# Performance work log

Measured on AMD Instinct MI355X. Metric: run time of the kernel, lower is better.

The kernel has to match this reference:

```python
import jax, jax.numpy as jnp
import numpy as np
from jax import lax

N, S, H, L, E, V = 10000, 20, 512, 2, 100000, 10000


def setup_inputs() -> dict:
    key = jax.random.key(0)
    ks = jax.random.split(key, 12)
    return {
        "emb": jax.random.normal(ks[0], (V, H), jnp.float32),
        "W_ir": jax.random.normal(ks[1], (L, H, H), jnp.float32) * (2.0 / H) ** 0.5,
        "b_ir": jnp.ones((L, H), jnp.float32),
        "W_iz": jax.random.normal(ks[2], (L, H, H), jnp.float32) * (2.0 / H) ** 0.5,
        "b_iz": jnp.ones((L, H), jnp.float32),
        "lin_w": jax.random.normal(ks[3], (1, H), jnp.float32) * (1.0 / H) ** 0.5,
        "lin_b": jnp.zeros((1,), jnp.float32),
        "skip_w": jax.random.uniform(ks[4], (H, H), jnp.float32),
        "skip_b": jax.random.uniform(ks[5], (H,), jnp.float32),
        "walk_idx": jax.random.randint(ks[6], (N, S), 0, V),
        "edge_label_index": jax.random.randint(ks[7], (2, E), 0, N),
    }


def reference(emb, W_ir, b_ir, W_iz, b_iz, lin_w, lin_b, skip_w, skip_b,
              walk_idx, edge_label_index):
    x = emb[walk_idx]                       # [N, S, H]
    hn = jnp.zeros((x.shape[0], emb.shape[1]), x.dtype)
    for l in range(W_ir.shape[0]):
        # gates depend only on x, precompute all steps: F.linear(x, W) = x @ W.T
        h_all = jnp.einsum('nsh,kh->snk', x, W_ir[l]) + b_ir[l]          # [S, N, H]
        z_all = jax.nn.sigmoid(jnp.einsum('nsh,kh->snk', x, W_iz[l]) + b_iz[l])

        def step(h, tz):
            ht, zt = tz
            return (1.0 - zt) * h + zt * ht, None

        hn, _ = lax.scan(step, hn, (h_all, z_all))
    # note: F.dropout result in original is dead (overwritten); omitted
    score = jax.nn.sigmoid(hn @ lin_w.T + lin_b)        # [N, 1]
    node_feat = score[edge_label_index]                  # [2, E, 1]
    pred = jnp.sum(node_feat[0] * node_feat[1], axis=-1)  # [E] ('dot' decode)
    out2 = hn @ skip_w.T + skip_b                        # [N, H]
    return pred, out2
```

## Files before the change

kernel.cpp:

```cpp
#include <hip/hip_runtime.h>

#define H  512
#define NN 10000
#define SS 20
#define VV 100000
#define EE 100000

typedef __bf16 bf16x8 __attribute__((ext_vector_type(8)));
typedef float  f32x4  __attribute__((ext_vector_type(4)));

__device__ __forceinline__ unsigned short f2bf(float f) {
  unsigned u = __builtin_bit_cast(unsigned, f);
  u += 0x7FFFu + ((u >> 16) & 1u);
  return (unsigned short)(u >> 16);
}
__device__ __forceinline__ float bflo(int x) {
  return __builtin_bit_cast(float, (unsigned)x << 16);
}
__device__ __forceinline__ float bfhi(int x) {
  return __builtin_bit_cast(float, (unsigned)x & 0xFFFF0000u);
}
__device__ __forceinline__ float sigm(float x) { return 1.f / (1.f + __expf(-x)); }

__device__ __forceinline__ unsigned pk(float lo, float hi) {
  unsigned a = __builtin_bit_cast(unsigned, lo) + 0x8000u;
  unsigned b = __builtin_bit_cast(unsigned, hi) + 0x8000u;
  return __builtin_amdgcn_perm(b, a, 0x07060302u);
}
__device__ __forceinline__ void cvt_store8(unsigned short* dst, float4 a, float4 b) {
  int4 v;
  v.x = (int)pk(a.x, a.y); v.y = (int)pk(a.z, a.w);
  v.z = (int)pk(b.x, b.y); v.w = (int)pk(b.z, b.w);
  *(int4*)dst = v;
}
__device__ __forceinline__ bf16x8 cvt8(float4 a, float4 b) {
  int4 v;
  v.x = (int)pk(a.x, a.y); v.y = (int)pk(a.z, a.w);
  v.z = (int)pk(b.x, b.y); v.w = (int)pk(b.z, b.w);
  return __builtin_bit_cast(bf16x8, v);
}

__launch_bounds__(256, 2)
__global__ void gru_fused(const float* __restrict__ emb,
                          const float* __restrict__ W_ir,
                          const float* __restrict__ W_iz,
                          const float* __restrict__ b_ir,
                          const float* __restrict__ b_iz,
                          const int* __restrict__ walk,
                          unsigned short* __restrict__ hnb) {
  __shared__ unsigned short As[2][80 * 64];
  __shared__ unsigned short hout[2][4][32];

  const int tid = threadIdx.x;
  const int w = tid >> 6, lane = tid & 63;
  const int r = lane & 15, q = lane >> 4;

  const int hwid = blockIdx.y * 16 + blockIdx.x;
  const int cg = (hwid >> 3) & 15;
  const int sb = ((hwid & 7) << 3) + (hwid >> 7);
  const int c0 = cg * 32;

  const int ly = r & 1;
  const int cch = c0 + 8 * w + (r >> 1);
  bf16x8 barr[2][16];
  float bias2[2];
  #pragma unroll
  for (int t = 0; t < 2; ++t) {
    const float* wrow = (t ? W_iz : W_ir) + (long)ly * H * H + (long)cch * H;
    #pragma unroll
    for (int u = 0; u < 16; ++u) {
      const float* s = wrow + u * 32 + q * 8;
      barr[t][u] = cvt8(*(const float4*)s, *(const float4*)(s + 4));
    }
    bias2[t] = (t ? b_iz : b_ir)[ly * H + cch];
  }

  const int row0 = tid >> 3, g0 = tid & 7;
  const int row1 = row0 + 32, row2 = row0 + 64;
  const bool has2 = (tid < 128);
  #define LMAP(m) (20 * (((m) >> 2) & 3) + 4 * ((m) >> 4) + ((m) & 3))
  #define SWZ(m)  ((m) * 64 + ((g0 ^ ((m) & 7)) * 8))
  const int L0 = LMAP(row0), L1 = LMAP(row1), L2 = LMAP(row2);
  const int sw0 = SWZ(row0), sw1 = SWZ(row1), sw2 = SWZ(row2);

  const int ngA = (2500 * sb) >> 6;
  const int ngB = (2500 * (sb + 1)) >> 6;

  int v0 = walk[ngA * 80 + L0]; v0 = ((unsigned)v0 < VV) ? v0 : 0;
  int v1 = walk[ngA * 80 + L1]; v1 = ((unsigned)v1 < VV) ? v1 : 0;
  int cur0 = v0 * H, cur1 = v1 * H, cur2 = 0;
  if (has2) { int v2 = walk[ngA * 80 + L2]; v2 = ((unsigned)v2 < VV) ? v2 : 0; cur2 = v2 * H; }

  float4 pa0, pb0, pa1, pb1, pa2 = {0,0,0,0}, pb2 = {0,0,0,0};
  {
    const float* s0 = emb + cur0 + g0 * 8;
    pa0 = *(const float4*)s0; pb0 = *(const float4*)(s0 + 4);
    const float* s1 = emb + cur1 + g0 * 8;
    pa1 = *(const float4*)s1; pb1 = *(const float4*)(s1 + 4);
    if (has2) { const float* s2 = emb + cur2 + g0 * 8;
                pa2 = *(const float4*)s2; pb2 = *(const float4*)(s2 + 4); }
  }

  f32x4 acc[5][2];
  const f32x4 fz = {0.f, 0.f, 0.f, 0.f};

  for (int ng = ngA; ng < ngB; ++ng) {
    #pragma unroll
    for (int mt = 0; mt < 5; ++mt)
      #pragma unroll
      for (int t = 0; t < 2; ++t) acc[mt][t] = fz;

    const int ngn = (ng + 1 < ngB) ? ng + 1 : ng;
    int n0 = walk[ngn * 80 + L0]; n0 = ((unsigned)n0 < VV) ? n0 : 0;
    int n1 = walk[ngn * 80 + L1]; n1 = ((unsigned)n1 < VV) ? n1 : 0;
    const int nxt0 = n0 * H, nxt1 = n1 * H;
    int nxt2 = 0;
    if (has2) { int n2 = walk[ngn * 80 + L2]; n2 = ((unsigned)n2 < VV) ? n2 : 0; nxt2 = n2 * H; }

    #pragma unroll
    for (int kc = 0; kc < 8; ++kc) {
      unsigned short* Ab = &As[kc & 1][0];
      cvt_store8(&Ab[sw0], pa0, pb0);
      cvt_store8(&Ab[sw1], pa1, pb1);
      if (has2) cvt_store8(&Ab[sw2], pa2, pb2);
      __syncthreads();
      {
        const int ko = (kc < 7) ? (kc + 1) * 64 : 0;
        const int o0 = (kc < 7) ? cur0 : nxt0;
        const int o1 = (kc < 7) ? cur1 : nxt1;
        const int o2 = (kc < 7) ? cur2 : nxt2;
        const float* s0 = emb + o0 + ko + g0 * 8;
        pa0 = *(const float4*)s0; pb0 = *(const float4*)(s0 + 4);
        const float* s1 = emb + o1 + ko + g0 * 8;
        pa1 = *(const float4*)s1; pb1 = *(const float4*)(s1 + 4);
        if (has2) { const float* s2 = emb + o2 + ko + g0 * 8;
                    pa2 = *(const float4*)s2; pb2 = *(const float4*)(s2 + 4); }
      }
      #pragma unroll
      for (int ks = 0; ks < 2; ++ks) {
        bf16x8 a[5];
        #pragma unroll
        for (int mt = 0; mt < 5; ++mt) {
          const int ar = mt * 16 + r;
          a[mt] = *(const bf16x8*)&Ab[ar * 64 + (((ks * 4 + q) ^ (ar & 7)) * 8)];
        }
        #pragma unroll
        for (int mt = 0; mt < 5; ++mt)
          #pragma unroll
          for (int t = 0; t < 2; ++t)
            acc[mt][t] = __builtin_amdgcn_mfma_f32_16x16x32_bf16(
                a[mt], barr[t][kc * 2 + ks], acc[mt][t], 0, 0, 0);
      }
    }

    {
      float hn1 = 0.f, a2 = 1.f, b2 = 0.f;
      #pragma unroll
      for (int s = 0; s < 20; ++s) {
        const float yh = acc[s >> 2][0][s & 3] + bias2[0];
        const float yz = acc[s >> 2][1][s & 3] + bias2[1];
        const float z = sigm(yz);
        hn1 += z * (yh - hn1);
        a2 *= (1.f - z);
        b2 += z * (yh - b2);
      }
      const float u2 = __shfl_xor(hn1, 1);
      if (ly == 1) hout[ng & 1][q][8 * w + (r >> 1)] = f2bf(a2 * u2 + b2);
    }
    __syncthreads();
    if (tid < 16) {
      const int nd = tid >> 2, seg = tid & 3;
      int4 v = *(const int4*)&hout[ng & 1][nd][seg * 8];
      *(int4*)(hnb + (long)(ng * 4 + nd) * 1024 + c0 + seg * 8) = v;
    }
    cur0 = nxt0; cur1 = nxt1; cur2 = nxt2;
  }
}

__global__ void score_kernel(const unsigned short* __restrict__ hnb,
                             const float* __restrict__ lin_w,
                             const float* __restrict__ lin_b,
                             float* __restrict__ R) {
  int tid = threadIdx.x;
  int wv = tid >> 6, lane = tid & 63;
  int node = blockIdx.x * 4 + wv;
  int k = lane * 8;
  int4 hv = *(const int4*)(hnb + (long)node * 1024 + k);
  float4 w0 = *(const float4*)(lin_w + k);
  float4 w1 = *(const float4*)(lin_w + k + 4);
  float s = bflo(hv.x) * w0.x + bfhi(hv.x) * w0.y + bflo(hv.y) * w0.z + bfhi(hv.y) * w0.w
          + bflo(hv.z) * w1.x + bfhi(hv.z) * w1.y + bflo(hv.w) * w1.z + bfhi(hv.w) * w1.w;
  #pragma unroll
  for (int off = 32; off > 0; off >>= 1) s += __shfl_down(s, off);
  if (lane == 0) R[256 + (long)node * 512] = sigm(s + lin_b[0]);
}

__global__ void pred_kernel(const int* __restrict__ eli, const float* __restrict__ R,
                            float* __restrict__ out) {
  int e = blockIdx.x * 256 + threadIdx.x;
  if (e < EE) {
    int a = eli[e];       a = (unsigned)a < NN ? a : 0;
    int b = eli[EE + e];  b = (unsigned)b < NN ? b : 0;
    out[e] = R[256 + (long)a * 512] * R[256 + (long)b * 512];
  }
}

__launch_bounds__(256)
__global__ void out2_kernel(const unsigned short* __restrict__ hnb,
                            const float* __restrict__ skip_w,
                            const float* __restrict__ skip_b,
                            float* __restrict__ out2) {
  __shared__ unsigned short Asl[32][520];
  __shared__ unsigned short Bsl[512][40];
  const int tid = threadIdx.x;
  const int lane = tid & 63, wv = tid >> 6;
  const int r = lane & 15, q = lane >> 4;
  const int m0 = blockIdx.x * 32;

  {
    int arow = tid >> 4;
    int acol = (tid & 15) * 32;
    #pragma unroll
    for (int hh = 0; hh < 2; ++hh) {
      int grow = m0 + hh * 16 + arow;
      unsigned short* dst = &Asl[hh * 16 + arow][acol];
      if (grow < NN) {
        const unsigned short* hr = hnb + (long)grow * 1024 + acol;
        *(int4*)(dst)      = *(const int4*)(hr);
        *(int4*)(dst + 8)  = *(const int4*)(hr + 8);
        *(int4*)(dst + 16) = *(const int4*)(hr + 16);
        *(int4*)(dst + 24) = *(const int4*)(hr + 24);
      } else {
        int4 z = {0, 0, 0, 0};
        *(int4*)(dst) = z; *(int4*)(dst + 8) = z;
        *(int4*)(dst + 16) = z; *(int4*)(dst + 24) = z;
      }
    }
  }

  const f32x4 fzero = {0.f, 0.f, 0.f, 0.f};
  f32x4 acc[2][8];
  #pragma unroll
  for (int rg = 0; rg < 2; ++rg)
    #pragma unroll
    for (int i = 0; i < 8; ++i) acc[rg][i] = fzero;

  const int ksub = (tid & 3) * 8;
  const int jb = tid >> 2;

  for (int k0 = 0; k0 < H; k0 += 32) {
    __syncthreads();
    #pragma unroll
    for (int it = 0; it < 8; ++it) {
      int jj = it * 64 + jb;
      const float* src = skip_w + (long)jj * H + k0 + ksub;
      cvt_store8(&Bsl[jj][ksub], *(const float4*)src, *(const float4*)(src + 4));
    }
    __syncthreads();
    bf16x8 af0 = *(const bf16x8*)&Asl[r][k0 + q * 8];
    bf16x8 af1 = *(const bf16x8*)&Asl[16 + r][k0 + q * 8];
    #pragma unroll
    for (int i = 0; i < 8; ++i) {
      bf16x8 bf = *(const bf16x8*)&Bsl[(wv * 8 + i) * 16 + r][q * 8];
      acc[0][i] = __builtin_amdgcn_mfma_f32_16x16x32_bf16(af0, bf, acc[0][i], 0, 0, 0);
      acc[1][i] = __builtin_amdgcn_mfma_f32_16x16x32_bf16(af1, bf, acc[1][i], 0, 0, 0);
    }
  }
  #pragma unroll
  for (int rg = 0; rg < 2; ++rg)
    #pragma unroll
    for (int i = 0; i < 8; ++i) {
      int col = (wv * 8 + i) * 16 + r;
      float sbv = skip_b[col];
      #pragma unroll
      for (int g = 0; g < 4; ++g) {
        int grow = m0 + rg * 16 + q * 4 + g;
        if (grow < NN) out2[(long)grow * H + col] = acc[rg][i][g] + sbv;
      }
    }
}

extern "C" void kernel_launch(void* const* d_in, const int* in_sizes, int n_in,
                              void* d_out, int out_size, void* d_ws, size_t ws_size,
                              hipStream_t stream) {
  const float* emb    = (const float*)d_in[0];
  const float* W_ir   = (const float*)d_in[1];
  const float* b_ir   = (const float*)d_in[2];
  const float* W_iz   = (const float*)d_in[3];
  const float* b_iz   = (const float*)d_in[4];
  const float* lin_w  = (const float*)d_in[5];
  const float* lin_b  = (const float*)d_in[6];
  const float* skip_w = (const float*)d_in[7];
  const float* skip_b = (const float*)d_in[8];
  const int*   walk   = (const int*)d_in[9];
  const int*   eli    = (const int*)d_in[10];
  float* out = (float*)d_out;
  float* R   = out + EE;
  unsigned short* hnb = (unsigned short*)R;

  dim3 g1(16, 64);
  gru_fused<<<g1, 256, 0, stream>>>(emb, W_ir, W_iz, b_ir, b_iz, walk, hnb);
  score_kernel<<<2500, 256, 0, stream>>>(hnb, lin_w, lin_b, R);
  pred_kernel<<<391, 256, 0, stream>>>(eli, R, out);
  out2_kernel<<<313, 256, 0, stream>>>(hnb, skip_w, skip_b, R);
}
```

Before: 778.5 us.

## Deepen gather pipeline to four LDS stages with two register prefetch slots

Replaces the double-buffered LDS staging of gathered embedding rows with a four-slot ring and two in-flight register prefetch sets, so global loads are issued three chunks ahead and LDS writes two chunks ahead of the MFMA consumer. __syncthreads is replaced by a custom barrier that waits only on LDS counters rather than on outstanding global loads, and MFMA sections are wrapped in s_setprio. The aim is to hide random-gather latency behind compute, at the cost of doubled LDS use and more registers, which may hurt the two-blocks-per-CU occupancy. The barrier choice depends on ring depth for correctness across iterations.

```diff
diff --git a/kernel.cpp b/kernel.cpp
--- a/kernel.cpp
+++ b/kernel.cpp
@@ -38,6 +38,10 @@
   v.x = (int)pk(a.x, a.y); v.y = (int)pk(a.z, a.w);
   v.z = (int)pk(b.x, b.y); v.w = (int)pk(b.z, b.w);
   return __builtin_bit_cast(bf16x8, v);
+}
+
+__device__ __forceinline__ void pub_barrier() {
+  asm volatile("s_waitcnt lgkmcnt(0)\n\ts_barrier" ::: "memory");
 }
 
 __launch_bounds__(256, 2)
@@ -48,7 +52,7 @@
                           const float* __restrict__ b_iz,
                           const int* __restrict__ walk,
                           unsigned short* __restrict__ hnb) {
-  __shared__ unsigned short As[2][80 * 64];
+  __shared__ unsigned short As[4][80 * 64];
   __shared__ unsigned short hout[2][4][32];
 
   const int tid = threadIdx.x;
@@ -91,14 +95,29 @@
   int cur0 = v0 * H, cur1 = v1 * H, cur2 = 0;
   if (has2) { int v2 = walk[ngA * 80 + L2]; v2 = ((unsigned)v2 < VV) ? v2 : 0; cur2 = v2 * H; }
 
-  float4 pa0, pb0, pa1, pb1, pa2 = {0,0,0,0}, pb2 = {0,0,0,0};
+  float4 p0a[2], p0b[2], p1a[2], p1b[2], p2a[2], p2b[2];
+  p2a[0] = p2a[1] = p2b[0] = p2b[1] = (float4){0, 0, 0, 0};
+
   {
     const float* s0 = emb + cur0 + g0 * 8;
-    pa0 = *(const float4*)s0; pb0 = *(const float4*)(s0 + 4);
     const float* s1 = emb + cur1 + g0 * 8;
-    pa1 = *(const float4*)s1; pb1 = *(const float4*)(s1 + 4);
-    if (has2) { const float* s2 = emb + cur2 + g0 * 8;
-                pa2 = *(const float4*)s2; pb2 = *(const float4*)(s2 + 4); }
+    const float* s2 = emb + cur2 + g0 * 8;
+    float4 a0 = *(const float4*)s0, b0 = *(const float4*)(s0 + 4);
+    float4 a1 = *(const float4*)s1, b1 = *(const float4*)(s1 + 4);
+    float4 a2 = {0,0,0,0}, b2 = {0,0,0,0};
+    if (has2) { a2 = *(const float4*)s2; b2 = *(const float4*)(s2 + 4); }
+    cvt_store8(&As[0][sw0], a0, b0);
+    cvt_store8(&As[0][sw1], a1, b1);
+    if (has2) cvt_store8(&As[0][sw2], a2, b2);
+    a0 = *(const float4*)(s0 + 64); b0 = *(const float4*)(s0 + 68);
+    a1 = *(const float4*)(s1 + 64); b1 = *(const float4*)(s1 + 68);
+    if (has2) { a2 = *(const float4*)(s2 + 64); b2 = *(const float4*)(s2 + 68); }
+    cvt_store8(&As[1][sw0], a0, b0);
+    cvt_store8(&As[1][sw1], a1, b1);
+    if (has2) cvt_store8(&As[1][sw2], a2, b2);
+    p0a[0] = *(const float4*)(s0 + 128); p0b[0] = *(const float4*)(s0 + 132);
+    p1a[0] = *(const float4*)(s1 + 128); p1b[0] = *(const float4*)(s1 + 132);
+    if (has2) { p2a[0] = *(const float4*)(s2 + 128); p2b[0] = *(const float4*)(s2 + 132); }
   }
 
   f32x4 acc[5][2];
@@ -119,23 +138,32 @@
 
     #pragma unroll
     for (int kc = 0; kc < 8; ++kc) {
-      unsigned short* Ab = &As[kc & 1][0];
-      cvt_store8(&Ab[sw0], pa0, pb0);
-      cvt_store8(&Ab[sw1], pa1, pb1);
-      if (has2) cvt_store8(&Ab[sw2], pa2, pb2);
-      __syncthreads();
+      pub_barrier();
+
       {
-        const int ko = (kc < 7) ? (kc + 1) * 64 : 0;
-        const int o0 = (kc < 7) ? cur0 : nxt0;
-        const int o1 = (kc < 7) ? cur1 : nxt1;
-        const int o2 = (kc < 7) ? cur2 : nxt2;
-        const float* s0 = emb + o0 + ko + g0 * 8;
-        pa0 = *(const float4*)s0; pb0 = *(const float4*)(s0 + 4);
-        const float* s1 = emb + o1 + ko + g0 * 8;
-        pa1 = *(const float4*)s1; pb1 = *(const float4*)(s1 + 4);
-        if (has2) { const float* s2 = emb + o2 + ko + g0 * 8;
-                    pa2 = *(const float4*)s2; pb2 = *(const float4*)(s2 + 4); }
-      }
+        const int cix = kc + 3;
+        const int off = (cix & 7) * 64;
+        const int u0 = (cix < 8) ? cur0 : nxt0;
+        const int u1 = (cix < 8) ? cur1 : nxt1;
+        const float* s0 = emb + u0 + off + g0 * 8;
+        p0a[cix & 1] = *(const float4*)s0; p0b[cix & 1] = *(const float4*)(s0 + 4);
+        const float* s1 = emb + u1 + off + g0 * 8;
+        p1a[cix & 1] = *(const float4*)s1; p1b[cix & 1] = *(const float4*)(s1 + 4);
+        if (has2) {
+          const int u2 = (cix < 8) ? cur2 : nxt2;
+          const float* s2 = emb + u2 + off + g0 * 8;
+          p2a[cix & 1] = *(const float4*)s2; p2b[cix & 1] = *(const float4*)(s2 + 4);
+        }
+      }
+
+      {
+        unsigned short* An = &As[(kc + 2) & 3][0];
+        cvt_store8(&An[sw0], p0a[kc & 1], p0b[kc & 1]);
+        cvt_store8(&An[sw1], p1a[kc & 1], p1b[kc & 1]);
+        if (has2) cvt_store8(&An[sw2], p2a[kc & 1], p2b[kc & 1]);
+      }
+
+      const unsigned short* Ab = &As[kc & 3][0];
       #pragma unroll
       for (int ks = 0; ks < 2; ++ks) {
         bf16x8 a[5];
@@ -144,12 +172,14 @@
           const int ar = mt * 16 + r;
           a[mt] = *(const bf16x8*)&Ab[ar * 64 + (((ks * 4 + q) ^ (ar & 7)) * 8)];
         }
+        __builtin_amdgcn_s_setprio(1);
         #pragma unroll
         for (int mt = 0; mt < 5; ++mt)
           #pragma unroll
           for (int t = 0; t < 2; ++t)
             acc[mt][t] = __builtin_amdgcn_mfma_f32_16x16x32_bf16(
                 a[mt], barr[t][kc * 2 + ks], acc[mt][t], 0, 0, 0);
+        __builtin_amdgcn_s_setprio(0);
       }
     }
 
@@ -167,7 +197,7 @@
       const float u2 = __shfl_xor(hn1, 1);
       if (ly == 1) hout[ng & 1][q][8 * w + (r >> 1)] = f2bf(a2 * u2 + b2);
     }
-    __syncthreads();
+    pub_barrier();
     if (tid < 16) {
       const int nd = tid >> 2, seg = tid & 3;
       int4 v = *(const int4*)&hout[ng & 1][nd][seg * 8];
```

Result: faster. 743.5 us (-4.5%).
